# Performance work log

Hardware: AMD Instinct MI355X
Metric: run time of the kernel (lower is better)

Reference implementation:

```python
import jax, jax.numpy as jnp
import numpy as np

EMBED_DIM = 768
NUM_HEADS = 12
HEAD_DIM = EMBED_DIM // NUM_HEADS
SEGMENT_LENGTHS = [2048, 4096, 8192]
DILATION_RATES = [1, 2, 4]
SCALE = 1.0 / np.sqrt(HEAD_DIM)
B, S = 1, 8192


def setup_inputs() -> dict:
    key = jax.random.key(0)
    ks = jax.random.split(key, 5)
    std = 1.0 / np.sqrt(EMBED_DIM)
    return {
        "x": jax.random.normal(ks[0], (B, S, EMBED_DIM), dtype=jnp.float32),
        "Wqkv": jax.random.normal(ks[1], (EMBED_DIM, 3 * EMBED_DIM), dtype=jnp.float32) * std,
        "bqkv": jax.random.normal(ks[2], (3 * EMBED_DIM,), dtype=jnp.float32) * 0.01,
        "Wout": jax.random.normal(ks[3], (EMBED_DIM, EMBED_DIM), dtype=jnp.float32) * std,
        "bout": jax.random.normal(ks[4], (EMBED_DIM,), dtype=jnp.float32) * 0.01,
    }


def _attend(q, k, v):
    # q,k,v: [B,H,L,D]; full softmax attention (non-causal)
    scores = jnp.einsum("bhqd,bhkd->bhqk", q, k) * SCALE
    w = jax.nn.softmax(scores, axis=-1)
    return jnp.einsum("bhqk,bhkd->bhqd", w, v)


def reference(x, Wqkv, bqkv, Wout, bout):
    b, s, _ = x.shape
    qkv = x @ Wqkv + bqkv                                  # [B,S,3E]
    qkv = qkv.reshape(b, s, 3, NUM_HEADS, HEAD_DIM)
    qkv = jnp.transpose(qkv, (2, 0, 3, 1, 4))              # [3,B,H,S,D]
    q, k, v = qkv[0], qkv[1], qkv[2]

    outputs = []
    for seg_len, dil in zip(SEGMENT_LENGTHS, DILATION_RATES):
        if seg_len > s:
            continue
        if dil > 1:
            idx = np.arange(0, s, dil)[:seg_len]           # static indices
            seg_out = _attend(q[:, :, idx, :], k[:, :, idx, :], v[:, :, idx, :])
            full = jnp.zeros((b, NUM_HEADS, s, HEAD_DIM), dtype=seg_out.dtype)
            full = full.at[:, :, idx, :].set(seg_out)
        else:
            seg_out = _attend(q[:, :, :seg_len, :], k[:, :, :seg_len, :], v[:, :, :seg_len, :])
            pad = s - seg_out.shape[2]
            full = jnp.pad(seg_out, ((0, 0), (0, 0), (0, pad), (0, 0))) if pad > 0 else seg_out
        outputs.append(full)

    out = jnp.mean(jnp.stack(outputs), axis=0) if len(outputs) > 1 else outputs[0]
    out = jnp.transpose(out, (0, 2, 1, 3)).reshape(b, s, EMBED_DIM)
    return out @ Wout + bout
```

## Files before the change

kernel.cpp:

```cpp
#include <hip/hip_runtime.h>
#include <hip/hip_bf16.h>

typedef float f32x4 __attribute__((ext_vector_type(4)));
typedef float fvec4 __attribute__((ext_vector_type(4)));
typedef __bf16 bf16x8 __attribute__((ext_vector_type(8)));
typedef __bf16 bf16x2 __attribute__((ext_vector_type(2)));

__device__ inline float fexp2(float x) {
#if __has_builtin(__builtin_amdgcn_exp2f)
    return __builtin_amdgcn_exp2f(x);
#else
    return exp2f(x);
#endif
}

__device__ __forceinline__ bf16x2 pk_bf16(float a, float b) {
#if __has_builtin(__builtin_amdgcn_cvt_pk_bf16_f32)
    auto t = __builtin_amdgcn_cvt_pk_bf16_f32(a, b);
    return __builtin_bit_cast(bf16x2, t);
#else
    bf16x2 r; r[0] = (__bf16)a; r[1] = (__bf16)b; return r;
#endif
}

#define MFMA_BF16(a, b, c) __builtin_amdgcn_mfma_f32_16x16x32_bf16((a), (b), (c), 0, 0, 0)
#define SCHED_FENCE() __builtin_amdgcn_sched_barrier(0)

__device__ __forceinline__ void gl2lds16(const void* g, void* l) {
    __builtin_amdgcn_global_load_lds((const __attribute__((address_space(1))) void*)g,
                                     (__attribute__((address_space(3))) void*)l, 16, 0, 0);
}

#define SEG1OFF ((size_t)12 * 2048 * 64)
#define SEG2OFF ((size_t)12 * 6144 * 64)
#define QSCALE 0.18033688f

__global__ __launch_bounds__(256) void prep_kernel(
    const float* __restrict__ x, const float* __restrict__ Wqkv,
    const float* __restrict__ Wout, __bf16* __restrict__ xb,
    __bf16* __restrict__ WqkvT, __bf16* __restrict__ WoutT) {
    int bid = blockIdx.x, tid = threadIdx.x;
    if (bid < 3072) {
        int i = bid * 256 + tid;
        fvec4 a = ((const fvec4*)x)[2 * i];
        fvec4 b = ((const fvec4*)x)[2 * i + 1];
        bf16x8 o;
        o[0] = (__bf16)a[0]; o[1] = (__bf16)a[1]; o[2] = (__bf16)a[2]; o[3] = (__bf16)a[3];
        o[4] = (__bf16)b[0]; o[5] = (__bf16)b[1]; o[6] = (__bf16)b[2]; o[7] = (__bf16)b[3];
        ((bf16x8*)xb)[i] = o;
    } else if (bid < 3936) {
        int b = bid - 3072;
        int n = (b % 9) * 256 + tid;
        int kg = b / 9;
        bf16x8 o;
#pragma unroll
        for (int j = 0; j < 8; j++) o[j] = (__bf16)Wqkv[(size_t)(kg * 8 + j) * 2304 + n];
        *(bf16x8*)&WqkvT[(size_t)n * 768 + kg * 8] = o;
    } else {
        int b = bid - 3936;
        int n = (b % 3) * 256 + tid;
        int kg = b / 3;
        bf16x8 o;
#pragma unroll
        for (int j = 0; j < 8; j++) o[j] = (__bf16)Wout[(size_t)(kg * 8 + j) * 768 + n];
        *(bf16x8*)&WoutT[(size_t)n * 768 + kg * 8] = o;
    }
}

__global__ __launch_bounds__(256, 2) void gemm_qkv_kernel(
    const __bf16* __restrict__ Ab, const __bf16* __restrict__ Bt,
    const float* __restrict__ bias,
    __bf16* __restrict__ Qc, __bf16* __restrict__ Kc, __bf16* __restrict__ Vt) {
    __shared__ __align__(16) char smem[65536];
    __bf16* T = (__bf16*)smem;
    int tid = threadIdx.x;
    int wave = tid >> 6, lane = tid & 63;
    int quad = lane >> 4, l15 = lane & 15;
    int bm = blockIdx.x * 128, bn = blockIdx.y * 128;
    int wm = (wave >> 1) * 64, wn = (wave & 1) * 64;
    int swzA = tid & 7;
    int rows_[4], chs_[4];
#pragma unroll
    for (int j = 0; j < 4; j++) {
        int s = j * 256 + tid;
        rows_[j] = s >> 3;
        chs_[j] = swzA ^ (rows_[j] & 7);
    }
    f32x4 acc[4][4] = {};
    {
#pragma unroll
        for (int j = 0; j < 4; j++) {
            gl2lds16(&Ab[(size_t)(bm + rows_[j]) * 768 + chs_[j] * 8],
                     smem + j * 4096 + wave * 1024);
            gl2lds16(&Bt[(size_t)(bn + rows_[j]) * 768 + chs_[j] * 8],
                     smem + 16384 + j * 4096 + wave * 1024);
        }
    }
    for (int ki = 0; ki < 12; ki++) {
        __syncthreads();
        int cur = ki & 1;
        if (ki + 1 < 12) {
            int nb = (cur ^ 1) * 32768;
            int k1 = (ki + 1) * 64;
#pragma unroll
            for (int j = 0; j < 4; j++) {
                gl2lds16(&Ab[(size_t)(bm + rows_[j]) * 768 + k1 + chs_[j] * 8],
                         smem + nb + j * 4096 + wave * 1024);
                gl2lds16(&Bt[(size_t)(bn + rows_[j]) * 768 + k1 + chs_[j] * 8],
                         smem + nb + 16384 + j * 4096 + wave * 1024);
            }
        }
        const __bf16* Al = (const __bf16*)(smem + cur * 32768);
        const __bf16* Bl = Al + 8192;
#pragma unroll
        for (int ks = 0; ks < 2; ks++) {
            bf16x8 af[4], bfr[4];
#pragma unroll
            for (int i = 0; i < 4; i++) {
                int row = wm + i * 16 + l15;
                af[i] = *(const bf16x8*)&Al[row * 64 + (((ks * 4 + quad) ^ (row & 7)) * 8)];
            }
#pragma unroll
            for (int j = 0; j < 4; j++) {
                int row = wn + j * 16 + l15;
                bfr[j] = *(const bf16x8*)&Bl[row * 64 + (((ks * 4 + quad) ^ (row & 7)) * 8)];
            }
#pragma unroll
            for (int i = 0; i < 4; i++)
#pragma unroll
                for (int j = 0; j < 4; j++)
                    acc[i][j] = MFMA_BF16(af[i], bfr[j], acc[i][j]);
        }
    }
    int which = blockIdx.y / 6;
    int h0 = (blockIdx.y % 6) * 2;
    float scl = which == 0 ? QSCALE : 1.0f;
    float bv[4];
#pragma unroll
    for (int j = 0; j < 4; j++) bv[j] = bias[bn + wn + j * 16 + l15];
    __syncthreads();
#pragma unroll
    for (int i = 0; i < 4; i++)
#pragma unroll
        for (int j = 0; j < 4; j++) {
            int col = wn + j * 16 + l15;
#pragma unroll
            for (int r = 0; r < 4; r++) {
                int row = wm + i * 16 + quad * 4 + r;
                int ch = ((col >> 3) & 8) | (((col >> 3) & 7) ^ (row & 7));
                T[row * 136 + ch * 8 + (col & 7)] =
                    (__bf16)((acc[i][j][r] + bv[j]) * scl);
            }
        }
    __syncthreads();
    if (which < 2) {
        __bf16* dst = which == 0 ? Qc : Kc;
        int rr = tid >> 4;
        int c8 = tid & 15;
        int hh = c8 >> 3, d8 = c8 & 7;
        int h = h0 + hh;
        __bf16* p0 = dst + ((size_t)h * 2048 * 64) + d8 * 8;
        __bf16* p1 = dst + SEG1OFF + ((size_t)h * 4096 * 64) + d8 * 8;
        __bf16* p2 = dst + SEG2OFF + ((size_t)h * 2048 * 64) + d8 * 8;
#pragma unroll
        for (int pass = 0; pass < 8; pass++) {
            int row = pass * 16 + rr;
            int pos = bm + row;
            int ch = (c8 & 8) | ((c8 & 7) ^ (row & 7));
            bf16x8 v = *(const bf16x8*)&T[row * 136 + ch * 8];
            if (pos < 2048) *(bf16x8*)&p0[(size_t)pos * 64] = v;
            if (!(pos & 1)) *(bf16x8*)&p1[(size_t)(pos >> 1) * 64] = v;
            if (!(pos & 3)) *(bf16x8*)&p2[(size_t)(pos >> 2) * 64] = v;
        }
    } else {
        {
            __bf16* base1 = Vt + SEG1OFF;
#pragma unroll
            for (int it = 0; it < 4; it++) {
                int sid = it * 256 + tid;
                int hh = sid >> 9, ck = (sid >> 6) & 7, d = sid & 63;
                int col = hh * 64 + d;
                int kb = (ck >> 2) * 32 + (ck & 3) * 4;
                bf16x8 o;
#pragma unroll
                for (int J = 0; J < 8; J++) {
                    int k = kb + (J & 3) + (J >> 2) * 16;
                    int r = 2 * k;
                    int sc = ((col >> 3) & 8) | (((col >> 3) & 7) ^ (r & 7));
                    o[J] = T[r * 136 + sc * 8 + (col & 7)];
                }
                *(bf16x8*)&base1[(size_t)(h0 + hh) * 64 * 4096 + (size_t)d * 4096 +
                                 (bm >> 1) + ck * 8] = o;
            }
        }
        if (bm < 2048) {
#pragma unroll
            for (int it = 0; it < 8; it++) {
                int sid = it * 256 + tid;
                int tsub = sid >> 10, rest = sid & 1023;
                int hh = rest >> 9, ck = (rest >> 6) & 7, d = rest & 63;
                int col = hh * 64 + d;
                int kb = (ck >> 2) * 32 + (ck & 3) * 4;
                bf16x8 o;
#pragma unroll
                for (int J = 0; J < 8; J++) {
                    int k = kb + (J & 3) + (J >> 2) * 16;
                    int r = tsub * 64 + k;
                    int sc = ((col >> 3) & 8) | (((col >> 3) & 7) ^ (r & 7));
                    o[J] = T[r * 136 + sc * 8 + (col & 7)];
                }
                *(bf16x8*)&Vt[(size_t)(h0 + hh) * 64 * 2048 + (size_t)d * 2048 +
                              bm + tsub * 64 + ck * 8] = o;
            }
        }
        {
            __bf16* base2 = Vt + SEG2OFF;
            int ckoff = (bm & 128) ? 4 : 0;
            int rsub = (bm & 128) ? 128 : 0;
#pragma unroll
            for (int it = 0; it < 2; it++) {
                int sid = it * 256 + tid;
                int hh = sid >> 8, cki = (sid >> 6) & 3, d = sid & 63;
                int ck = cki + ckoff;
                int col = hh * 64 + d;
                int kb = (ck >> 2) * 32 + (ck & 3) * 4;
                bf16x8 o;
#pragma unroll
                for (int J = 0; J < 8; J++) {
                    int k = kb + (J & 3) + (J >> 2) * 16;
                    int r = 4 * k - rsub;
                    int sc = ((col >> 3) & 8) | (((col >> 3) & 7) ^ (r & 7));
                    o[J] = T[r * 136 + sc * 8 + (col & 7)];
                }
                *(bf16x8*)&base2[(size_t)(h0 + hh) * 64 * 2048 + (size_t)d * 2048 +
                                 (bm >> 8) * 64 + ck * 8] = o;
            }
        }
    }
}

__global__ __launch_bounds__(256) void gemm_out_kernel(
    const __bf16* __restrict__ Ab, const __bf16* __restrict__ Bt,
    const float* __restrict__ bias, float* __restrict__ Co) {
    __shared__ __align__(16) char smem[49152];
    int tid = threadIdx.x;
    int wave = tid >> 6, lane = tid & 63;
    int quad = lane >> 4, l15 = lane & 15;
    int bm = blockIdx.x * 64, bn = blockIdx.y * 128;
    int wn = wave * 32;
    int rowsA[2], chsA[2], rowsB[4], chsB[4];
#pragma unroll
    for (int j = 0; j < 2; j++) {
        int s = j * 256 + tid;
        rowsA[j] = s >> 3;
        chsA[j] = (s & 7) ^ (rowsA[j] & 7);
    }
#pragma unroll
    for (int j = 0; j < 4; j++) {
        int s = j * 256 + tid;
        rowsB[j] = s >> 3;
        chsB[j] = (s & 7) ^ (rowsB[j] & 7);
    }
    f32x4 acc[4][2] = {};
    {
#pragma unroll
        for (int j = 0; j < 2; j++)
            gl2lds16(&Ab[(size_t)(bm + rowsA[j]) * 768 + chsA[j] * 8],
                     smem + j * 4096 + wave * 1024);
#pragma unroll
        for (int j = 0; j < 4; j++)
            gl2lds16(&Bt[(size_t)(bn + rowsB[j]) * 768 + chsB[j] * 8],
                     smem + 8192 + j * 4096 + wave * 1024);
    }
    for (int ki = 0; ki < 12; ki++) {
        __syncthreads();
        int cur = ki & 1;
        if (ki + 1 < 12) {
            int nb = (cur ^ 1) * 24576;
            int k1 = (ki + 1) * 64;
#pragma unroll
            for (int j = 0; j < 2; j++)
                gl2lds16(&Ab[(size_t)(bm + rowsA[j]) * 768 + k1 + chsA[j] * 8],
                         smem + nb + j * 4096 + wave * 1024);
#pragma unroll
            for (int j = 0; j < 4; j++)
                gl2lds16(&Bt[(size_t)(bn + rowsB[j]) * 768 + k1 + chsB[j] * 8],
                         smem + nb + 8192 + j * 4096 + wave * 1024);
        }
        const __bf16* Al = (const __bf16*)(smem + cur * 24576);
        const __bf16* Bl = Al + 4096;
#pragma unroll
        for (int ks = 0; ks < 2; ks++) {
            bf16x8 af[4], bfr[2];
#pragma unroll
            for (int i = 0; i < 4; i++) {
                int row = i * 16 + l15;
                af[i] = *(const bf16x8*)&Al[row * 64 + (((ks * 4 + quad) ^ (row & 7)) * 8)];
            }
#pragma unroll
            for (int j = 0; j < 2; j++) {
                int row = wn + j * 16 + l15;
                bfr[j] = *(const bf16x8*)&Bl[row * 64 + (((ks * 4 + quad) ^ (row & 7)) * 8)];
            }
#pragma unroll
            for (int i = 0; i < 4; i++)
#pragma unroll
                for (int j = 0; j < 2; j++)
                    acc[i][j] = MFMA_BF16(af[i], bfr[j], acc[i][j]);
        }
    }
#pragma unroll
    for (int j = 0; j < 2; j++) {
        int c = bn + wn + j * 16 + l15;
        float bv = bias[c];
#pragma unroll
        for (int i = 0; i < 4; i++)
#pragma unroll
            for (int r = 0; r < 4; r++) {
                int row = bm + i * 16 + quad * 4 + r;
                Co[(size_t)row * 768 + c] = acc[i][j][r] + bv;
            }
    }
}

__global__ __launch_bounds__(256, 2) void attn_kernel(
    const __bf16* __restrict__ Qcb, const __bf16* __restrict__ Kcb,
    const __bf16* __restrict__ Vtb,
    float* __restrict__ O0, float* __restrict__ O1a, float* __restrict__ O1b,
    float* __restrict__ O1c, float* __restrict__ O1d, float* __restrict__ O2,
    float* __restrict__ L0, float* __restrict__ L1a, float* __restrict__ L1b,
    float* __restrict__ L1c, float* __restrict__ L1d, float* __restrict__ L2) {
    __shared__ __bf16 Kl[2 * 4096];
    __shared__ __bf16 Vl[2 * 4096];
    int bid = blockIdx.x;
    int seg, piece = 0, head, qt, Lc, iters;
    if (bid < 192)      { seg = 0; head = bid % 12; qt = bid / 12; Lc = 2048; iters = 32; }
    else if (bid < 384) { int i = bid - 192; seg = 2; head = i % 12; qt = i / 12; Lc = 2048; iters = 32; }
    else                { int i = bid - 384; seg = 1; head = i % 12; int rest = i / 12;
                          qt = rest >> 2; piece = rest & 3; Lc = 4096; iters = 16; }
    size_t soff = seg == 0 ? 0 : (seg == 1 ? SEG1OFF : SEG2OFF);
    const __bf16* Qh = Qcb + soff + (size_t)head * Lc * 64;
    const __bf16* Kh = Kcb + soff + (size_t)head * Lc * 64;
    const __bf16* Vh = Vtb + soff + (size_t)head * 64 * Lc;
    float* Ob;
    float* Lb;
    if (seg == 0)      { Ob = O0; Lb = L0 + head * 2048; }
    else if (seg == 2) { Ob = O2; Lb = L2 + head * 2048; }
    else {
        Ob = piece == 0 ? O1a : (piece == 1 ? O1b : (piece == 2 ? O1c : O1d));
        Lb = (piece == 0 ? L1a : (piece == 1 ? L1b : (piece == 2 ? L1c : L1d))) + head * 4096;
    }
    int kvb = piece * 16;
    int tid = threadIdx.x, wave = tid >> 6, lane = tid & 63;
    int quad = lane >> 4, l15 = lane & 15;
    bf16x8 qf[2][2];
#pragma unroll
    for (int qg = 0; qg < 2; qg++) {
        size_t qpos = (size_t)(qt * 128 + wave * 32 + qg * 16 + l15);
        qf[qg][0] = *(const bf16x8*)&Qh[qpos * 64 + quad * 8];
        qf[qg][1] = *(const bf16x8*)&Qh[qpos * 64 + 32 + quad * 8];
    }
    f32x4 o[2][4] = {};
    f32x4 lacc[2] = {};
    bf16x8 ones;
#pragma unroll
    for (int j = 0; j < 8; j++) ones[j] = (__bf16)1.0f;
    int kv0 = tid >> 3, cl0 = tid & 7;
    int kdb0 = cl0 ^ (kv0 & 7);
    int kv1 = kv0 + 32, kdb1 = cl0 ^ (kv1 & 7);
    char* KlB = (char*)Kl;
    char* VlB = (char*)Vl;
    int swz = l15 & 7;
    {
        int t0 = kvb * 64;
        gl2lds16(&Kh[(size_t)(t0 + kv0) * 64 + kdb0 * 8], KlB + wave * 1024);
        gl2lds16(&Kh[(size_t)(t0 + kv1) * 64 + kdb1 * 8], KlB + 4096 + wave * 1024);
        SCHED_FENCE();
        gl2lds16(&Vh[(size_t)kv0 * Lc + t0 + kdb0 * 8], VlB + wave * 1024);
        gl2lds16(&Vh[(size_t)kv1 * Lc + t0 + kdb1 * 8], VlB + 4096 + wave * 1024);
    }
    for (int nt = 0; nt < iters; nt++) {
        int cur = nt & 1;
        SCHED_FENCE();
        asm volatile("s_waitcnt vmcnt(2)" ::: "memory");
        __builtin_amdgcn_s_barrier();
        SCHED_FENCE();
        if (nt + 1 < iters) {
            int nb = 8192 * (cur ^ 1);
            int t1 = (kvb + nt + 1) * 64;
            gl2lds16(&Kh[(size_t)(t1 + kv0) * 64 + kdb0 * 8], KlB + nb + wave * 1024);
            gl2lds16(&Kh[(size_t)(t1 + kv1) * 64 + kdb1 * 8], KlB + nb + 4096 + wave * 1024);
            SCHED_FENCE();
            gl2lds16(&Vh[(size_t)kv0 * Lc + t1 + kdb0 * 8], VlB + nb + wave * 1024);
            gl2lds16(&Vh[(size_t)kv1 * Lc + t1 + kdb1 * 8], VlB + nb + 4096 + wave * 1024);
        }
        SCHED_FENCE();
        const __bf16* Kt = Kl + cur * 4096;
        const __bf16* Vt_ = Vl + cur * 4096;
        f32x4 sarr[4][2];
        __builtin_amdgcn_s_setprio(1);
#pragma unroll
        for (int c = 0; c < 4; c++) {
            int krow = (c * 16 + l15) * 64;
            bf16x8 kf0 = *(const bf16x8*)&Kt[krow + ((quad ^ swz) * 8)];
            bf16x8 kf1 = *(const bf16x8*)&Kt[krow + (((4 + quad) ^ swz) * 8)];
#pragma unroll
            for (int qg = 0; qg < 2; qg++) {
                f32x4 z = {};
                z = MFMA_BF16(kf0, qf[qg][0], z);
                sarr[c][qg] = MFMA_BF16(kf1, qf[qg][1], z);
            }
        }
        __builtin_amdgcn_s_setprio(0);
        union { bf16x8 v8; bf16x2 v2[4]; } pf8[2][2];
#pragma unroll
        for (int qg = 0; qg < 2; qg++)
#pragma unroll
            for (int c = 0; c < 4; c++) {
                float p0 = fexp2(sarr[c][qg][0]);
                float p1 = fexp2(sarr[c][qg][1]);
                float p2 = fexp2(sarr[c][qg][2]);
                float p3 = fexp2(sarr[c][qg][3]);
                pf8[qg][c >> 1].v2[(c & 1) * 2 + 0] = pk_bf16(p0, p1);
                pf8[qg][c >> 1].v2[(c & 1) * 2 + 1] = pk_bf16(p2, p3);
            }
        SCHED_FENCE();
        if (nt + 1 < iters) {
            asm volatile("s_waitcnt vmcnt(4)" ::: "memory");
        } else {
            asm volatile("s_waitcnt vmcnt(0)" ::: "memory");
        }
        __builtin_amdgcn_s_barrier();
        SCHED_FENCE();
        __builtin_amdgcn_s_setprio(1);
#pragma unroll
        for (int u = 0; u < 2; u++) {
#pragma unroll
            for (int ds = 0; ds < 4; ds++) {
                int d = ds * 16 + l15;
                bf16x8 vf = *(const bf16x8*)&Vt_[d * 64 + (((u * 4 + quad) ^ swz) * 8)];
                o[0][ds] = MFMA_BF16(vf, pf8[0][u].v8, o[0][ds]);
                o[1][ds] = MFMA_BF16(vf, pf8[1][u].v8, o[1][ds]);
            }
            lacc[0] = MFMA_BF16(ones, pf8[0][u].v8, lacc[0]);
            lacc[1] = MFMA_BF16(ones, pf8[1][u].v8, lacc[1]);
        }
        __builtin_amdgcn_s_setprio(0);
    }
#pragma unroll
    for (int qg = 0; qg < 2; qg++) {
        float l = lacc[qg][0];
        int pos = qt * 128 + wave * 32 + qg * 16 + l15;
        float* orow = Ob + (size_t)pos * 768 + head * 64;
#pragma unroll
        for (int ds = 0; ds < 4; ds++)
            *(f32x4*)&orow[ds * 16 + quad * 4] = o[qg][ds];
        if (lane < 16) Lb[qt * 128 + wave * 32 + qg * 16 + lane] = l;
    }
}

__global__ __launch_bounds__(256) void combine_kernel(
    const float* __restrict__ O0, const float* __restrict__ O1a,
    const float* __restrict__ O1b, const float* __restrict__ O1c,
    const float* __restrict__ O1d, const float* __restrict__ O2,
    const float* __restrict__ L0, const float* __restrict__ L1a,
    const float* __restrict__ L1b, const float* __restrict__ L1c,
    const float* __restrict__ L1d, const float* __restrict__ L2,
    __bf16* __restrict__ attnF) {
    int g = blockIdx.x * 256 + threadIdx.x;
    int q = g / 96;
    int cs = (g - q * 96) * 8;
    int head = cs >> 6;
    f32x4 a0 = {}, a1 = {};
    if (q < 2048) {
        float inv = 1.0f / L0[head * 2048 + q];
        const f32x4* p = (const f32x4*)&O0[(size_t)q * 768 + cs];
        a0 += p[0] * inv; a1 += p[1] * inv;
    }
    if (!(q & 1)) {
        int p1 = q >> 1;
        int li = head * 4096 + p1;
        float inv = 1.0f / (L1a[li] + L1b[li] + L1c[li] + L1d[li]);
        size_t ro = (size_t)p1 * 768 + cs;
        const f32x4* pa = (const f32x4*)&O1a[ro];
        const f32x4* pb = (const f32x4*)&O1b[ro];
        const f32x4* pc = (const f32x4*)&O1c[ro];
        const f32x4* pd = (const f32x4*)&O1d[ro];
        a0 += ((pa[0] + pb[0]) + (pc[0] + pd[0])) * inv;
        a1 += ((pa[1] + pb[1]) + (pc[1] + pd[1])) * inv;
    }
    if (!(q & 3)) {
        int p2 = q >> 2;
        float inv = 1.0f / L2[head * 2048 + p2];
        const f32x4* p = (const f32x4*)&O2[(size_t)p2 * 768 + cs];
        a0 += p[0] * inv; a1 += p[1] * inv;
    }
    const float third = 1.0f / 3.0f;
    bf16x8 ov;
    ov[0] = (__bf16)(a0[0] * third); ov[1] = (__bf16)(a0[1] * third);
    ov[2] = (__bf16)(a0[2] * third); ov[3] = (__bf16)(a0[3] * third);
    ov[4] = (__bf16)(a1[0] * third); ov[5] = (__bf16)(a1[1] * third);
    ov[6] = (__bf16)(a1[2] * third); ov[7] = (__bf16)(a1[3] * third);
    *(bf16x8*)&attnF[(size_t)q * 768 + cs] = ov;
}

extern "C" void kernel_launch(void* const* d_in, const int* in_sizes, int n_in,
                              void* d_out, int out_size, void* d_ws, size_t ws_size,
                              hipStream_t stream) {
    const float* x    = (const float*)d_in[0];
    const float* Wqkv = (const float*)d_in[1];
    const float* bqkv = (const float*)d_in[2];
    const float* Wout = (const float*)d_in[3];
    const float* bout = (const float*)d_in[4];
    float* out = (float*)d_out;
    (void)in_sizes; (void)n_in; (void)out_size; (void)ws_size;

    char* ws = (char*)d_ws;
    size_t off = 0;
    auto take = [&](size_t bytes) -> void* {
        void* p = ws + off;
        off += (bytes + 255) & ~(size_t)255;
        return p;
    };
    const size_t QKV_ELEMS = (size_t)12 * 8192 * 64;
    __bf16* xb    = (__bf16*)take((size_t)8192 * 768 * 2);
    __bf16* WqkvT = (__bf16*)take((size_t)2304 * 768 * 2);
    __bf16* WoutT = (__bf16*)take((size_t)768 * 768 * 2);
    __bf16* Qc    = (__bf16*)take(QKV_ELEMS * 2);
    __bf16* Kc    = (__bf16*)take(QKV_ELEMS * 2);
    __bf16* Vc    = (__bf16*)take(QKV_ELEMS * 2);
    __bf16* Vt    = (__bf16*)take(QKV_ELEMS * 2);
    float*  O1a   = (float*)take((size_t)4096 * 768 * 4);
    float*  O1b   = (float*)take((size_t)4096 * 768 * 4);
    float*  O1c   = (float*)take((size_t)4096 * 768 * 4);
    float*  L0    = (float*)take((size_t)12 * 2048 * 4);
    float*  L1a   = (float*)take((size_t)12 * 4096 * 4);
    float*  L1b   = (float*)take((size_t)12 * 4096 * 4);
    float*  L1c   = (float*)take((size_t)12 * 4096 * 4);
    float*  L1d   = (float*)take((size_t)12 * 4096 * 4);
    float*  L2    = (float*)take((size_t)12 * 2048 * 4);
    float*  O0    = (float*)xb;
    float*  O2    = O0 + (size_t)2048 * 768;
    float*  O1d   = (float*)Vc;
    __bf16* attnF = Qc;

    prep_kernel<<<4224, 256, 0, stream>>>(x, Wqkv, Wout, xb, WqkvT, WoutT);
    gemm_qkv_kernel<<<dim3(64, 18), 256, 0, stream>>>(xb, WqkvT, bqkv, Qc, Kc, Vt);
    attn_kernel<<<1920, 256, 0, stream>>>(Qc, Kc, Vt, O0, O1a, O1b, O1c, O1d, O2,
                                          L0, L1a, L1b, L1c, L1d, L2);
    combine_kernel<<<3072, 256, 0, stream>>>(O0, O1a, O1b, O1c, O1d, O2,
                                             L0, L1a, L1b, L1c, L1d, L2, attnF);
    gemm_out_kernel<<<dim3(128, 6), 256, 0, stream>>>(attnF, WoutT, bout, out);
}
```

Measured before the change: 243.4 us.

## Double query rows per attention block to reuse K/V tiles across more queries

Each attention block now handles 256 query rows (64 per wave, four 16-row groups) instead of 128, halving the grid to 960 blocks and halving K/V global-to-LDS traffic per query. Block-to-work mapping is reordered so the query tiles of one head sit next to each other. The exp/pack step now runs per key chunk, interleaved with the QK^T MFMAs, which may shorten score register lifetimes. The cost is more accumulator registers per wave and fewer blocks, which could lower occupancy or leave CUs unevenly loaded.

Measured after the change: 247.3 us. Within noise of the previous version (+1.6%).

```diff
diff --git a/kernel.cpp b/kernel.cpp
--- a/kernel.cpp
+++ b/kernel.cpp
@@ -334,10 +334,10 @@
     __shared__ __bf16 Vl[2 * 4096];
     int bid = blockIdx.x;
     int seg, piece = 0, head, qt, Lc, iters;
-    if (bid < 192)      { seg = 0; head = bid % 12; qt = bid / 12; Lc = 2048; iters = 32; }
-    else if (bid < 384) { int i = bid - 192; seg = 2; head = i % 12; qt = i / 12; Lc = 2048; iters = 32; }
-    else                { int i = bid - 384; seg = 1; head = i % 12; int rest = i / 12;
-                          qt = rest >> 2; piece = rest & 3; Lc = 4096; iters = 16; }
+    if (bid < 96)       { seg = 0; head = bid >> 3; qt = bid & 7; Lc = 2048; iters = 32; }
+    else if (bid < 192) { int i = bid - 96; seg = 2; head = i >> 3; qt = i & 7; Lc = 2048; iters = 32; }
+    else                { int i = bid - 192; seg = 1; head = i >> 6; int r = i & 63;
+                          qt = r >> 2; piece = r & 3; Lc = 4096; iters = 16; }
     size_t soff = seg == 0 ? 0 : (seg == 1 ? SEG1OFF : SEG2OFF);
     const __bf16* Qh = Qcb + soff + (size_t)head * Lc * 64;
     const __bf16* Kh = Kcb + soff + (size_t)head * Lc * 64;
@@ -353,15 +353,15 @@
     int kvb = piece * 16;
     int tid = threadIdx.x, wave = tid >> 6, lane = tid & 63;
     int quad = lane >> 4, l15 = lane & 15;
-    bf16x8 qf[2][2];
-#pragma unroll
-    for (int qg = 0; qg < 2; qg++) {
-        size_t qpos = (size_t)(qt * 128 + wave * 32 + qg * 16 + l15);
+    bf16x8 qf[4][2];
+#pragma unroll
+    for (int qg = 0; qg < 4; qg++) {
+        size_t qpos = (size_t)(qt * 256 + wave * 64 + qg * 16 + l15);
         qf[qg][0] = *(const bf16x8*)&Qh[qpos * 64 + quad * 8];
         qf[qg][1] = *(const bf16x8*)&Qh[qpos * 64 + 32 + quad * 8];
     }
-    f32x4 o[2][4] = {};
-    f32x4 lacc[2] = {};
+    f32x4 o[4][4] = {};
+    f32x4 lacc[4] = {};
     bf16x8 ones;
 #pragma unroll
     for (int j = 0; j < 8; j++) ones[j] = (__bf16)1.0f;
@@ -397,33 +397,31 @@
         SCHED_FENCE();
         const __bf16* Kt = Kl + cur * 4096;
         const __bf16* Vt_ = Vl + cur * 4096;
-        f32x4 sarr[4][2];
+        union { bf16x8 v8; bf16x2 v2[4]; } pf8[4][2];
         __builtin_amdgcn_s_setprio(1);
 #pragma unroll
         for (int c = 0; c < 4; c++) {
             int krow = (c * 16 + l15) * 64;
             bf16x8 kf0 = *(const bf16x8*)&Kt[krow + ((quad ^ swz) * 8)];
             bf16x8 kf1 = *(const bf16x8*)&Kt[krow + (((4 + quad) ^ swz) * 8)];
-#pragma unroll
-            for (int qg = 0; qg < 2; qg++) {
+            f32x4 s[4];
+#pragma unroll
+            for (int qg = 0; qg < 4; qg++) {
                 f32x4 z = {};
                 z = MFMA_BF16(kf0, qf[qg][0], z);
-                sarr[c][qg] = MFMA_BF16(kf1, qf[qg][1], z);
-            }
-        }
-        __builtin_amdgcn_s_setprio(0);
-        union { bf16x8 v8; bf16x2 v2[4]; } pf8[2][2];
-#pragma unroll
-        for (int qg = 0; qg < 2; qg++)
-#pragma unroll
-            for (int c = 0; c < 4; c++) {
-                float p0 = fexp2(sarr[c][qg][0]);
-                float p1 = fexp2(sarr[c][qg][1]);
-                float p2 = fexp2(sarr[c][qg][2]);
-                float p3 = fexp2(sarr[c][qg][3]);
+                s[qg] = MFMA_BF16(kf1, qf[qg][1], z);
+            }
+#pragma unroll
+            for (int qg = 0; qg < 4; qg++) {
+                float p0 = fexp2(s[qg][0]);
+                float p1 = fexp2(s[qg][1]);
+                float p2 = fexp2(s[qg][2]);
+                float p3 = fexp2(s[qg][3]);
                 pf8[qg][c >> 1].v2[(c & 1) * 2 + 0] = pk_bf16(p0, p1);
                 pf8[qg][c >> 1].v2[(c & 1) * 2 + 1] = pk_bf16(p2, p3);
             }
+        }
+        __builtin_amdgcn_s_setprio(0);
         SCHED_FENCE();
         if (nt + 1 < iters) {
             asm volatile("s_waitcnt vmcnt(4)" ::: "memory");
@@ -439,23 +437,25 @@
             for (int ds = 0; ds < 4; ds++) {
                 int d = ds * 16 + l15;
                 bf16x8 vf = *(const bf16x8*)&Vt_[d * 64 + (((u * 4 + quad) ^ swz) * 8)];
-                o[0][ds] = MFMA_BF16(vf, pf8[0][u].v8, o[0][ds]);
-                o[1][ds] = MFMA_BF16(vf, pf8[1][u].v8, o[1][ds]);
-            }
-            lacc[0] = MFMA_BF16(ones, pf8[0][u].v8, lacc[0]);
-            lacc[1] = MFMA_BF16(ones, pf8[1][u].v8, lacc[1]);
+#pragma unroll
+                for (int qg = 0; qg < 4; qg++)
+                    o[qg][ds] = MFMA_BF16(vf, pf8[qg][u].v8, o[qg][ds]);
+            }
+#pragma unroll
+            for (int qg = 0; qg < 4; qg++)
+                lacc[qg] = MFMA_BF16(ones, pf8[qg][u].v8, lacc[qg]);
         }
         __builtin_amdgcn_s_setprio(0);
     }
 #pragma unroll
-    for (int qg = 0; qg < 2; qg++) {
+    for (int qg = 0; qg < 4; qg++) {
         float l = lacc[qg][0];
-        int pos = qt * 128 + wave * 32 + qg * 16 + l15;
+        int pos = qt * 256 + wave * 64 + qg * 16 + l15;
         float* orow = Ob + (size_t)pos * 768 + head * 64;
 #pragma unroll
         for (int ds = 0; ds < 4; ds++)
             *(f32x4*)&orow[ds * 16 + quad * 4] = o[qg][ds];
-        if (lane < 16) Lb[qt * 128 + wave * 32 + qg * 16 + lane] = l;
+        if (lane < 16) Lb[pos] = l;
     }
 }
 
@@ -546,8 +546,8 @@
 
     prep_kernel<<<4224, 256, 0, stream>>>(x, Wqkv, Wout, xb, WqkvT, WoutT);
     gemm_qkv_kernel<<<dim3(64, 18), 256, 0, stream>>>(xb, WqkvT, bqkv, Qc, Kc, Vt);
-    attn_kernel<<<1920, 256, 0, stream>>>(Qc, Kc, Vt, O0, O1a, O1b, O1c, O1d, O2,
-                                          L0, L1a, L1b, L1c, L1d, L2);
+    attn_kernel<<<960, 256, 0, stream>>>(Qc, Kc, Vt, O0, O1a, O1b, O1c, O1d, O2,
+                                         L0, L1a, L1b, L1c, L1d, L2);
     combine_kernel<<<3072, 256, 0, stream>>>(O0, O1a, O1b, O1c, O1d, O2,
                                              L0, L1a, L1b, L1c, L1d, L2, attnF);
     gemm_out_kernel<<<dim3(128, 6), 256, 0, stream>>>(attnF, WoutT, bout, out);
```
